# Kernel optimization log

Hardware: AMD Instinct MI355X
Metric: run time of the kernel (lower is better)

Reference implementation:

```python
import jax, jax.numpy as jnp
import numpy as np

D_KEY = 512
D_VALUE = 512
D_MEM_HIDDEN = 64
BATCH = 65536


def setup_inputs() -> dict:
    key = jax.random.key(0)
    ks = jax.random.split(key, 6)
    return {
        "key": jax.random.normal(ks[0], (BATCH, D_KEY), dtype=jnp.float32),
        "value": jax.random.normal(ks[1], (BATCH, D_VALUE), dtype=jnp.float32),
        # memory MLP weights (the stored memory)
        "mem_W1": jax.random.normal(ks[2], (D_MEM_HIDDEN, D_KEY), dtype=jnp.float32) * 0.02,
        "mem_b1": jnp.zeros((D_MEM_HIDDEN,), dtype=jnp.float32),
        "mem_W2": jax.random.normal(ks[3], (D_VALUE, D_MEM_HIDDEN), dtype=jnp.float32) * 0.02,
        "mem_b2": jnp.zeros((D_VALUE,), dtype=jnp.float32),
        # per-dimension precision head
        "prec_W": jax.random.normal(ks[4], (D_VALUE, D_KEY), dtype=jnp.float32) * 0.01,
        "prec_b": jnp.ones((D_VALUE,), dtype=jnp.float32),
    }


def reference(key, value, mem_W1, mem_b1, mem_W2, mem_b2, prec_W, prec_b):
    """Faithful translation of MemoryModule.free_energy.

    F = prec * clamp(value - pred, -3, 3)^2 - log(prec), averaged over d_value.
    """
    # predict: two-layer MLP with exact (erf) GELU, matching torch F.gelu default
    h = jax.nn.gelu(key @ mem_W1.T + mem_b1, approximate=False)  # (B, H)
    pred = h @ mem_W2.T + mem_b2                                  # (B, Dv)
    # precision head: softplus + 0.01, always positive
    prec = jax.nn.softplus(key @ prec_W.T + prec_b) + 0.01        # (B, Dv)
    error = jnp.clip(value - pred, -3.0, 3.0)                     # (B, Dv)
    F_per_dim = prec * error * error - jnp.log(prec)
    F_scalar = F_per_dim.mean(axis=-1)                            # (B,)
    return (F_scalar, pred, prec, error)
```

## Files before the change

kernel.cpp:

```cpp
#include <hip/hip_runtime.h>
#include <hip/hip_bf16.h>

#define BATCH 65536
#define DK 512
#define DV 512
#define DH 64
#define BMR 16

typedef __attribute__((ext_vector_type(8))) short bf16x8;
typedef __attribute__((ext_vector_type(4))) float f32x4;

__device__ __align__(16) short g_wb[327680];

__device__ __forceinline__ short f2bf(float f) {
    union { __hip_bfloat16 h; short s; } u;
    u.h = __float2bfloat16(f);
    return u.s;
}

__device__ __forceinline__ bf16x8 pack8(float4 a, float4 b) {
    bf16x8 r;
    r[0] = f2bf(a.x); r[1] = f2bf(a.y); r[2] = f2bf(a.z); r[3] = f2bf(a.w);
    r[4] = f2bf(b.x); r[5] = f2bf(b.y); r[6] = f2bf(b.z); r[7] = f2bf(b.w);
    return r;
}

__global__ __launch_bounds__(256) void conv_weights(
    const float* __restrict__ W1, const float* __restrict__ W2,
    const float* __restrict__ Wp)
{
    int f = blockIdx.x * 256 + threadIdx.x;
    int lane = f & 63;
    const float* src; int stride, row, col;
    if (f < 4096) {
        int t = f >> 10, kk = (f >> 6) & 15;
        src = W1; stride = DK;
        row = t * 16 + (lane & 15); col = kk * 32 + (lane >> 4) * 8;
    } else if (f < 8192) {
        int g = f - 4096; int t = g >> 7, kh = (g >> 6) & 1;
        src = W2; stride = DH;
        row = t * 16 + (lane & 15); col = kh * 32 + (lane >> 4) * 8;
    } else {
        int g = f - 8192; int t = g >> 10, kk = (g >> 6) & 15;
        src = Wp; stride = DK;
        row = t * 16 + (lane & 15); col = kk * 32 + (lane >> 4) * 8;
    }
    const float* p = src + (long)row * stride + col;
    float4 a = *reinterpret_cast<const float4*>(p);
    float4 b = *reinterpret_cast<const float4*>(p + 4);
    *reinterpret_cast<bf16x8*>(g_wb + (long)f * 8) = pack8(a, b);
}

#define KOF 0
#define XP  16384
#define XZ  24576

__global__ __launch_bounds__(256, 4) void fused_free_energy(
    const float* __restrict__ key, const float* __restrict__ value,
    const float* __restrict__ b1, const float* __restrict__ b2,
    const float* __restrict__ pb,
    float* __restrict__ outF, float* __restrict__ outPred,
    float* __restrict__ outPrec, float* __restrict__ outErr)
{
    __shared__ __align__(16) char lds[32768];

    const bf16x8* W1F = reinterpret_cast<const bf16x8*>(g_wb);
    const bf16x8* W2F = reinterpret_cast<const bf16x8*>(g_wb + 32768);
    const bf16x8* WpF = reinterpret_cast<const bf16x8*>(g_wb + 65536);

    const int tid  = threadIdx.x;
    const int wave = tid >> 6;
    const int lane = tid & 63;
    const int lh   = lane & 15;
    const int lg   = lane >> 4;
    const long row0 = (long)blockIdx.x * BMR;
    const f32x4 zf = {0.f, 0.f, 0.f, 0.f};

    {
        #pragma unroll
        for (int i = 0; i < 4; ++i) {
            int idx = i * 256 + tid;
            int r = idx >> 6, c8 = idx & 63;
            const float* p = key + (row0 + r) * DK + c8 * 8;
            float4 a = *reinterpret_cast<const float4*>(p);
            float4 b = *reinterpret_cast<const float4*>(p + 4);
            int byte = (r * 1024 + c8 * 16) ^ ((r & 7) << 4);
            *reinterpret_cast<bf16x8*>(lds + KOF + byte) = pack8(a, b);
        }
    }
    __syncthreads();

    #define KFRAG(kk) (*reinterpret_cast<const bf16x8*>( \
        lds + KOF + ((lh * 1024 + (kk) * 64 + lg * 16) ^ ((lh & 7) << 4))))

    bf16x8 hreg[2];
    {
        short hs_all[16];
        #pragma unroll
        for (int jt = 0; jt < 4; ++jt) {
            f32x4 aE = zf, aO = zf;
            #pragma unroll
            for (int kk = 0; kk < 16; kk += 2) {
                bf16x8 f0 = W1F[(jt * 16 + kk) * 64 + lane];
                bf16x8 f1 = W1F[(jt * 16 + kk + 1) * 64 + lane];
                aE = __builtin_amdgcn_mfma_f32_16x16x32_bf16(f0, KFRAG(kk),     aE, 0, 0, 0);
                aO = __builtin_amdgcn_mfma_f32_16x16x32_bf16(f1, KFRAG(kk + 1), aO, 0, 0, 0);
            }
            float4 b1v = *reinterpret_cast<const float4*>(b1 + jt * 16 + lg * 4);
            float b1a[4] = {b1v.x, b1v.y, b1v.z, b1v.w};
            #pragma unroll
            for (int r = 0; r < 4; ++r) {
                float z = aE[r] + aO[r] + b1a[r];
                float g = 0.5f * z * (1.0f + erff(z * 0.70710678f));
                hs_all[jt * 4 + r] = f2bf(g);
            }
        }
        #pragma unroll
        for (int jt = 0; jt < 4; ++jt) {
            int hb = XP + wave * 2048 + ((lh * 128 + jt * 32 + lg * 8) ^ ((lh & 7) << 4));
            short4 hv = {hs_all[jt * 4 + 0], hs_all[jt * 4 + 1],
                         hs_all[jt * 4 + 2], hs_all[jt * 4 + 3]};
            *reinterpret_cast<short4*>(lds + hb) = hv;
        }
        __syncthreads();
        #pragma unroll
        for (int kh = 0; kh < 2; ++kh) {
            int byte = (lh * 128 + kh * 64 + lg * 16) ^ ((lh & 7) << 4);
            hreg[kh] = *reinterpret_cast<const bf16x8*>(lds + XP + wave * 2048 + byte);
        }
        __syncthreads();
    }

    float facc0 = 0.f, facc1 = 0.f;
    #pragma unroll 1
    for (int ot = 0; ot < 4; ++ot) {
        #pragma unroll
        for (int sub = 0; sub < 2; ++sub) {
            const int tt = ot * 8 + wave * 2 + sub;
            f32x4 aE = zf, aO = zf;
            #pragma unroll
            for (int kk = 0; kk < 16; kk += 2) {
                bf16x8 f0 = WpF[(tt * 16 + kk) * 64 + lane];
                bf16x8 f1 = WpF[(tt * 16 + kk + 1) * 64 + lane];
                aE = __builtin_amdgcn_mfma_f32_16x16x32_bf16(f0, KFRAG(kk),     aE, 0, 0, 0);
                aO = __builtin_amdgcn_mfma_f32_16x16x32_bf16(f1, KFRAG(kk + 1), aO, 0, 0, 0);
            }
            f32x4 acc2 = zf;
            #pragma unroll
            for (int kh = 0; kh < 2; ++kh) {
                bf16x8 f = W2F[(tt * 2 + kh) * 64 + lane];
                acc2 = __builtin_amdgcn_mfma_f32_16x16x32_bf16(f, hreg[kh], acc2, 0, 0, 0);
            }
            int nb = tt * 16 + lg * 4;
            float4 b2v = *reinterpret_cast<const float4*>(b2 + nb);
            float4 pbv = *reinterpret_cast<const float4*>(pb + nb);
            f32x4 pz, zz;
            pz[0] = acc2[0] + b2v.x; pz[1] = acc2[1] + b2v.y;
            pz[2] = acc2[2] + b2v.z; pz[3] = acc2[3] + b2v.w;
            zz[0] = aE[0] + aO[0] + pbv.x; zz[1] = aE[1] + aO[1] + pbv.y;
            zz[2] = aE[2] + aO[2] + pbv.z; zz[3] = aE[3] + aO[3] + pbv.w;
            int relb = (wave * 2 + sub) * 64 + lg * 16;
            int sb = (lh * 512 + relb) ^ ((lh & 7) << 4);
            *reinterpret_cast<f32x4*>(lds + XP + sb) = pz;
            *reinterpret_cast<f32x4*>(lds + XZ + sb) = zz;
        }
        __syncthreads();

        #pragma unroll
        for (int ch = 0; ch < 2; ++ch) {
            int row  = wave * 4 + (lane >> 5) + ch * 2;
            int colb = (lane & 31) * 16;
            int rb   = (row * 512 + colb) ^ ((row & 7) << 4);
            float4 pr = *reinterpret_cast<const float4*>(lds + XP + rb);
            float4 zz = *reinterpret_cast<const float4*>(lds + XZ + rb);
            long ga = (row0 + row) * (long)DV + ot * 128 + (lane & 31) * 4;
            float4 va = *reinterpret_cast<const float4*>(value + ga);
            float pa[4] = {pr.x, pr.y, pr.z, pr.w};
            float za[4] = {zz.x, zz.y, zz.z, zz.w};
            float vaa[4] = {va.x, va.y, va.z, va.w};
            float er[4], pc[4], f = 0.f;
            #pragma unroll
            for (int r = 0; r < 4; ++r) {
                float z = za[r];
                float prec = fmaxf(z, 0.f) + __logf(1.0f + __expf(-fabsf(z))) + 0.01f;
                float e = fminf(fmaxf(vaa[r] - pa[r], -3.f), 3.f);
                pc[r] = prec; er[r] = e;
                f += prec * e * e - __logf(prec);
            }
            float4 pc4 = {pc[0], pc[1], pc[2], pc[3]};
            float4 er4 = {er[0], er[1], er[2], er[3]};
            *reinterpret_cast<float4*>(outPred + ga) = pr;
            *reinterpret_cast<float4*>(outPrec + ga) = pc4;
            *reinterpret_cast<float4*>(outErr  + ga) = er4;
            if (ch == 0) facc0 += f; else facc1 += f;
        }
        __syncthreads();
    }

    #pragma unroll
    for (int ch = 0; ch < 2; ++ch) {
        float s = (ch == 0) ? facc0 : facc1;
        #pragma unroll
        for (int off = 1; off < 32; off <<= 1)
            s += __shfl_xor(s, off, 64);
        if ((lane & 31) == 0)
            outF[row0 + wave * 4 + (lane >> 5) + ch * 2] = s * (1.0f / 512.0f);
    }
}

extern "C" void kernel_launch(void* const* d_in, const int* in_sizes, int n_in,
                              void* d_out, int out_size, void* d_ws, size_t ws_size,
                              hipStream_t stream) {
    const float* key   = (const float*)d_in[0];
    const float* value = (const float*)d_in[1];
    const float* W1    = (const float*)d_in[2];
    const float* b1    = (const float*)d_in[3];
    const float* W2    = (const float*)d_in[4];
    const float* b2    = (const float*)d_in[5];
    const float* Wp    = (const float*)d_in[6];
    const float* pb    = (const float*)d_in[7];

    float* outF    = (float*)d_out;
    float* outPred = outF + BATCH;
    float* outPrec = outPred + (long)BATCH * DV;
    float* outErr  = outPrec + (long)BATCH * DV;

    conv_weights<<<160, 256, 0, stream>>>(W1, W2, Wp);
    fused_free_energy<<<BATCH / BMR, 256, 0, stream>>>(key, value, b1, b2, pb,
                                                       outF, outPred, outPrec, outErr);
}
```

Measured before the change: 272.1 us.

## Prefetch value tiles one stage ahead and replace syncthreads with lighter barriers

Loads the value rows for the next output tile into registers before computing the current tile, so global load latency overlaps the MFMA work. The four-stage loop is fully unrolled with a double-buffered register prefetch. __syncthreads is replaced by an explicit s_waitcnt lgkmcnt(0) plus s_barrier, so barriers no longer wait on outstanding global memory operations. This uses more registers, and the barrier after the writeback has no explicit waitcnt, which relies on the LDS reads having already completed when their results were consumed.

```diff
diff --git a/kernel.cpp b/kernel.cpp
--- a/kernel.cpp
+++ b/kernel.cpp
@@ -9,6 +9,11 @@
 
 typedef __attribute__((ext_vector_type(8))) short bf16x8;
 typedef __attribute__((ext_vector_type(4))) float f32x4;
+
+#define LGKM_BAR() do { asm volatile("s_waitcnt lgkmcnt(0)" ::: "memory"); \
+                        __builtin_amdgcn_s_barrier(); } while (0)
+#define BAR()      do { asm volatile("" ::: "memory"); \
+                        __builtin_amdgcn_s_barrier(); } while (0)
 
 __device__ __align__(16) short g_wb[327680];
 
@@ -76,6 +81,18 @@
     const long row0 = (long)blockIdx.x * BMR;
     const f32x4 zf = {0.f, 0.f, 0.f, 0.f};
 
+    const int rowA  = wave * 4 + (lane >> 5);
+    const int colw  = (lane & 31) * 4;
+    const float* vbase0 = value + (row0 + rowA) * (long)DV + colw;
+    const float* vbase1 = vbase0 + 2 * DV;
+
+    float4 vA0, vA1, vB0, vB1;
+#define PREF(p, d0, d1) do { \
+        d0 = *reinterpret_cast<const float4*>(vbase0 + (p) * 128); \
+        d1 = *reinterpret_cast<const float4*>(vbase1 + (p) * 128); } while (0)
+
+    PREF(0, vA0, vA1);
+
     {
         #pragma unroll
         for (int i = 0; i < 4; ++i) {
@@ -88,7 +105,7 @@
             *reinterpret_cast<bf16x8*>(lds + KOF + byte) = pack8(a, b);
         }
     }
-    __syncthreads();
+    LGKM_BAR();
 
     #define KFRAG(kk) (*reinterpret_cast<const bf16x8*>( \
         lds + KOF + ((lh * 1024 + (kk) * 64 + lg * 16) ^ ((lh & 7) << 4))))
@@ -122,80 +139,92 @@
                          hs_all[jt * 4 + 2], hs_all[jt * 4 + 3]};
             *reinterpret_cast<short4*>(lds + hb) = hv;
         }
-        __syncthreads();
+        LGKM_BAR();
         #pragma unroll
         for (int kh = 0; kh < 2; ++kh) {
             int byte = (lh * 128 + kh * 64 + lg * 16) ^ ((lh & 7) << 4);
             hreg[kh] = *reinterpret_cast<const bf16x8*>(lds + XP + wave * 2048 + byte);
         }
-        __syncthreads();
+        LGKM_BAR();
     }
 
     float facc0 = 0.f, facc1 = 0.f;
-    #pragma unroll 1
-    for (int ot = 0; ot < 4; ++ot) {
-        #pragma unroll
-        for (int sub = 0; sub < 2; ++sub) {
-            const int tt = ot * 8 + wave * 2 + sub;
-            f32x4 aE = zf, aO = zf;
-            #pragma unroll
-            for (int kk = 0; kk < 16; kk += 2) {
-                bf16x8 f0 = WpF[(tt * 16 + kk) * 64 + lane];
-                bf16x8 f1 = WpF[(tt * 16 + kk + 1) * 64 + lane];
-                aE = __builtin_amdgcn_mfma_f32_16x16x32_bf16(f0, KFRAG(kk),     aE, 0, 0, 0);
-                aO = __builtin_amdgcn_mfma_f32_16x16x32_bf16(f1, KFRAG(kk + 1), aO, 0, 0, 0);
-            }
-            f32x4 acc2 = zf;
-            #pragma unroll
-            for (int kh = 0; kh < 2; ++kh) {
-                bf16x8 f = W2F[(tt * 2 + kh) * 64 + lane];
-                acc2 = __builtin_amdgcn_mfma_f32_16x16x32_bf16(f, hreg[kh], acc2, 0, 0, 0);
-            }
-            int nb = tt * 16 + lg * 4;
-            float4 b2v = *reinterpret_cast<const float4*>(b2 + nb);
-            float4 pbv = *reinterpret_cast<const float4*>(pb + nb);
-            f32x4 pz, zz;
-            pz[0] = acc2[0] + b2v.x; pz[1] = acc2[1] + b2v.y;
-            pz[2] = acc2[2] + b2v.z; pz[3] = acc2[3] + b2v.w;
-            zz[0] = aE[0] + aO[0] + pbv.x; zz[1] = aE[1] + aO[1] + pbv.y;
-            zz[2] = aE[2] + aO[2] + pbv.z; zz[3] = aE[3] + aO[3] + pbv.w;
-            int relb = (wave * 2 + sub) * 64 + lg * 16;
-            int sb = (lh * 512 + relb) ^ ((lh & 7) << 4);
-            *reinterpret_cast<f32x4*>(lds + XP + sb) = pz;
-            *reinterpret_cast<f32x4*>(lds + XZ + sb) = zz;
-        }
-        __syncthreads();
-
-        #pragma unroll
-        for (int ch = 0; ch < 2; ++ch) {
-            int row  = wave * 4 + (lane >> 5) + ch * 2;
-            int colb = (lane & 31) * 16;
-            int rb   = (row * 512 + colb) ^ ((row & 7) << 4);
-            float4 pr = *reinterpret_cast<const float4*>(lds + XP + rb);
-            float4 zz = *reinterpret_cast<const float4*>(lds + XZ + rb);
-            long ga = (row0 + row) * (long)DV + ot * 128 + (lane & 31) * 4;
-            float4 va = *reinterpret_cast<const float4*>(value + ga);
-            float pa[4] = {pr.x, pr.y, pr.z, pr.w};
-            float za[4] = {zz.x, zz.y, zz.z, zz.w};
-            float vaa[4] = {va.x, va.y, va.z, va.w};
-            float er[4], pc[4], f = 0.f;
-            #pragma unroll
-            for (int r = 0; r < 4; ++r) {
-                float z = za[r];
-                float prec = fmaxf(z, 0.f) + __logf(1.0f + __expf(-fabsf(z))) + 0.01f;
-                float e = fminf(fmaxf(vaa[r] - pa[r], -3.f), 3.f);
-                pc[r] = prec; er[r] = e;
-                f += prec * e * e - __logf(prec);
-            }
-            float4 pc4 = {pc[0], pc[1], pc[2], pc[3]};
-            float4 er4 = {er[0], er[1], er[2], er[3]};
-            *reinterpret_cast<float4*>(outPred + ga) = pr;
-            *reinterpret_cast<float4*>(outPrec + ga) = pc4;
-            *reinterpret_cast<float4*>(outErr  + ga) = er4;
-            if (ch == 0) facc0 += f; else facc1 += f;
-        }
-        __syncthreads();
-    }
+
+#define COMPUTE(ot) do {                                                          \
+        _Pragma("unroll")                                                         \
+        for (int sub = 0; sub < 2; ++sub) {                                       \
+            const int tt = (ot) * 8 + wave * 2 + sub;                             \
+            f32x4 aE = zf, aO = zf;                                               \
+            _Pragma("unroll")                                                     \
+            for (int kk = 0; kk < 16; kk += 2) {                                  \
+                bf16x8 f0 = WpF[(tt * 16 + kk) * 64 + lane];                      \
+                bf16x8 f1 = WpF[(tt * 16 + kk + 1) * 64 + lane];                  \
+                aE = __builtin_amdgcn_mfma_f32_16x16x32_bf16(f0, KFRAG(kk),     aE, 0, 0, 0); \
+                aO = __builtin_amdgcn_mfma_f32_16x16x32_bf16(f1, KFRAG(kk + 1), aO, 0, 0, 0); \
+            }                                                                     \
+            f32x4 acc2 = zf;                                                      \
+            _Pragma("unroll")                                                     \
+            for (int kh = 0; kh < 2; ++kh) {                                      \
+                bf16x8 f = W2F[(tt * 2 + kh) * 64 + lane];                        \
+                acc2 = __builtin_amdgcn_mfma_f32_16x16x32_bf16(f, hreg[kh], acc2, 0, 0, 0); \
+            }                                                                     \
+            int nb = tt * 16 + lg * 4;                                            \
+            float4 b2v = *reinterpret_cast<const float4*>(b2 + nb);               \
+            float4 pbv = *reinterpret_cast<const float4*>(pb + nb);               \
+            f32x4 pz, zz;                                                         \
+            pz[0] = acc2[0] + b2v.x; pz[1] = acc2[1] + b2v.y;                     \
+            pz[2] = acc2[2] + b2v.z; pz[3] = acc2[3] + b2v.w;                     \
+            zz[0] = aE[0] + aO[0] + pbv.x; zz[1] = aE[1] + aO[1] + pbv.y;         \
+            zz[2] = aE[2] + aO[2] + pbv.z; zz[3] = aE[3] + aO[3] + pbv.w;         \
+            int relb = (wave * 2 + sub) * 64 + lg * 16;                           \
+            int sb = (lh * 512 + relb) ^ ((lh & 7) << 4);                         \
+            *reinterpret_cast<f32x4*>(lds + XP + sb) = pz;                        \
+            *reinterpret_cast<f32x4*>(lds + XZ + sb) = zz;                        \
+        }                                                                         \
+    } while (0)
+
+#define WRITEBACK(ot, v0, v1) do {                                                \
+        _Pragma("unroll")                                                         \
+        for (int ch = 0; ch < 2; ++ch) {                                          \
+            int row  = rowA + ch * 2;                                             \
+            int colb = (lane & 31) * 16;                                          \
+            int rb   = (row * 512 + colb) ^ ((row & 7) << 4);                     \
+            float4 pr = *reinterpret_cast<const float4*>(lds + XP + rb);          \
+            float4 zv = *reinterpret_cast<const float4*>(lds + XZ + rb);          \
+            long ga = (row0 + row) * (long)DV + (ot) * 128 + colw;                \
+            float4 va = (ch == 0) ? (v0) : (v1);                                  \
+            float pa[4]  = {pr.x, pr.y, pr.z, pr.w};                              \
+            float za[4]  = {zv.x, zv.y, zv.z, zv.w};                              \
+            float vaa[4] = {va.x, va.y, va.z, va.w};                              \
+            float er[4], pc[4], f = 0.f;                                          \
+            _Pragma("unroll")                                                     \
+            for (int r = 0; r < 4; ++r) {                                         \
+                float z = za[r];                                                  \
+                float prec = fmaxf(z, 0.f) + __logf(1.0f + __expf(-fabsf(z))) + 0.01f; \
+                float e = fminf(fmaxf(vaa[r] - pa[r], -3.f), 3.f);                \
+                pc[r] = prec; er[r] = e;                                          \
+                f += prec * e * e - __logf(prec);                                 \
+            }                                                                     \
+            float4 pc4 = {pc[0], pc[1], pc[2], pc[3]};                            \
+            float4 er4 = {er[0], er[1], er[2], er[3]};                            \
+            *reinterpret_cast<float4*>(outPred + ga) = pr;                        \
+            *reinterpret_cast<float4*>(outPrec + ga) = pc4;                       \
+            *reinterpret_cast<float4*>(outErr  + ga) = er4;                       \
+            if (ch == 0) facc0 += f; else facc1 += f;                             \
+        }                                                                         \
+    } while (0)
+
+    COMPUTE(0); PREF(1, vB0, vB1); LGKM_BAR();
+    WRITEBACK(0, vA0, vA1); BAR();
+
+    COMPUTE(1); PREF(2, vA0, vA1); LGKM_BAR();
+    WRITEBACK(1, vB0, vB1); BAR();
+
+    COMPUTE(2); PREF(3, vB0, vB1); LGKM_BAR();
+    WRITEBACK(2, vA0, vA1); BAR();
+
+    COMPUTE(3); LGKM_BAR();
+    WRITEBACK(3, vB0, vB1);
 
     #pragma unroll
     for (int ch = 0; ch < 2; ++ch) {
@@ -204,7 +233,7 @@
         for (int off = 1; off < 32; off <<= 1)
             s += __shfl_xor(s, off, 64);
         if ((lane & 31) == 0)
-            outF[row0 + wave * 4 + (lane >> 5) + ch * 2] = s * (1.0f / 512.0f);
+            outF[row0 + rowA + ch * 2] = s * (1.0f / 512.0f);
     }
 }
 
```

Measured after the change: 261.3 us. 1.04x faster.

## Double row tile to 32 so each weight fragment feeds two MFMAs

Applied to the files above, without the earlier changes.

Raises the block row tile from 16 to 32 rows. Each loaded precision-head and W2 weight fragment is now reused across two M-tiles, which halves the global or L2 weight traffic per row. The W1/GELU stage runs on only two waves, the value loads are hoisted to the top of each phase, plain barriers are replaced with an lgkmcnt-wait plus s_barrier, and the final F reduction now goes through LDS. The cost is more LDS per block (48KB) and an occupancy hint lowered to 3 blocks per CU, with half the waves idle during the hidden-layer stage.

```diff
diff --git a/kernel.cpp b/kernel.cpp
--- a/kernel.cpp
+++ b/kernel.cpp
@@ -5,10 +5,13 @@
 #define DK 512
 #define DV 512
 #define DH 64
-#define BMR 16
+#define BMR 32
 
 typedef __attribute__((ext_vector_type(8))) short bf16x8;
 typedef __attribute__((ext_vector_type(4))) float f32x4;
+
+#define LGKM_BAR() do { asm volatile("s_waitcnt lgkmcnt(0)" ::: "memory"); \
+                        __builtin_amdgcn_s_barrier(); } while (0)
 
 __device__ __align__(16) short g_wb[327680];
 
@@ -52,17 +55,17 @@
 }
 
 #define KOF 0
-#define XP  16384
-#define XZ  24576
-
-__global__ __launch_bounds__(256, 4) void fused_free_energy(
+#define XP  32768
+#define XZ  40960
+
+__global__ __launch_bounds__(256, 3) void fused_free_energy(
     const float* __restrict__ key, const float* __restrict__ value,
     const float* __restrict__ b1, const float* __restrict__ b2,
     const float* __restrict__ pb,
     float* __restrict__ outF, float* __restrict__ outPred,
     float* __restrict__ outPrec, float* __restrict__ outErr)
 {
-    __shared__ __align__(16) char lds[32768];
+    __shared__ __align__(16) char lds[49152];
 
     const bf16x8* W1F = reinterpret_cast<const bf16x8*>(g_wb);
     const bf16x8* W2F = reinterpret_cast<const bf16x8*>(g_wb + 32768);
@@ -76,26 +79,27 @@
     const long row0 = (long)blockIdx.x * BMR;
     const f32x4 zf = {0.f, 0.f, 0.f, 0.f};
 
-    {
-        #pragma unroll
-        for (int i = 0; i < 4; ++i) {
-            int idx = i * 256 + tid;
-            int r = idx >> 6, c8 = idx & 63;
-            const float* p = key + (row0 + r) * DK + c8 * 8;
-            float4 a = *reinterpret_cast<const float4*>(p);
-            float4 b = *reinterpret_cast<const float4*>(p + 4);
-            int byte = (r * 1024 + c8 * 16) ^ ((r & 7) << 4);
-            *reinterpret_cast<bf16x8*>(lds + KOF + byte) = pack8(a, b);
-        }
-    }
-    __syncthreads();
-
-    #define KFRAG(kk) (*reinterpret_cast<const bf16x8*>( \
-        lds + KOF + ((lh * 1024 + (kk) * 64 + lg * 16) ^ ((lh & 7) << 4))))
-
-    bf16x8 hreg[2];
-    {
-        short hs_all[16];
+    const int rw = tid >> 4;
+    const int cw = (tid & 15) * 4;
+    const float* vrow0 = value + (row0 + rw) * (long)DV + cw;
+    const float* vrow1 = vrow0 + 16 * (long)DV;
+
+    #pragma unroll
+    for (int i = 0; i < 8; ++i) {
+        int idx = i * 256 + tid;
+        int r = idx >> 6, c8 = idx & 63;
+        const float* p = key + (row0 + r) * DK + c8 * 8;
+        float4 a = *reinterpret_cast<const float4*>(p);
+        float4 b = *reinterpret_cast<const float4*>(p + 4);
+        int byte = (r * 1024 + c8 * 16) ^ ((r & 7) << 4);
+        *reinterpret_cast<bf16x8*>(lds + KOF + byte) = pack8(a, b);
+    }
+    LGKM_BAR();
+
+    #define KFRAG(mt, kk) (*reinterpret_cast<const bf16x8*>( \
+        lds + KOF + (((mt) * 16384 + lh * 1024 + (kk) * 64 + lg * 16) ^ ((lh & 7) << 4))))
+
+    if (wave < 2) {
         #pragma unroll
         for (int jt = 0; jt < 4; ++jt) {
             f32x4 aE = zf, aO = zf;
@@ -103,80 +107,94 @@
             for (int kk = 0; kk < 16; kk += 2) {
                 bf16x8 f0 = W1F[(jt * 16 + kk) * 64 + lane];
                 bf16x8 f1 = W1F[(jt * 16 + kk + 1) * 64 + lane];
-                aE = __builtin_amdgcn_mfma_f32_16x16x32_bf16(f0, KFRAG(kk),     aE, 0, 0, 0);
-                aO = __builtin_amdgcn_mfma_f32_16x16x32_bf16(f1, KFRAG(kk + 1), aO, 0, 0, 0);
+                aE = __builtin_amdgcn_mfma_f32_16x16x32_bf16(f0, KFRAG(wave, kk),     aE, 0, 0, 0);
+                aO = __builtin_amdgcn_mfma_f32_16x16x32_bf16(f1, KFRAG(wave, kk + 1), aO, 0, 0, 0);
             }
             float4 b1v = *reinterpret_cast<const float4*>(b1 + jt * 16 + lg * 4);
             float b1a[4] = {b1v.x, b1v.y, b1v.z, b1v.w};
+            short hs[4];
             #pragma unroll
             for (int r = 0; r < 4; ++r) {
                 float z = aE[r] + aO[r] + b1a[r];
                 float g = 0.5f * z * (1.0f + erff(z * 0.70710678f));
-                hs_all[jt * 4 + r] = f2bf(g);
+                hs[r] = f2bf(g);
             }
-        }
-        #pragma unroll
-        for (int jt = 0; jt < 4; ++jt) {
             int hb = XP + wave * 2048 + ((lh * 128 + jt * 32 + lg * 8) ^ ((lh & 7) << 4));
-            short4 hv = {hs_all[jt * 4 + 0], hs_all[jt * 4 + 1],
-                         hs_all[jt * 4 + 2], hs_all[jt * 4 + 3]};
+            short4 hv = {hs[0], hs[1], hs[2], hs[3]};
             *reinterpret_cast<short4*>(lds + hb) = hv;
         }
-        __syncthreads();
+    }
+    LGKM_BAR();
+    bf16x8 hreg[2][2];
+    #pragma unroll
+    for (int mt = 0; mt < 2; ++mt)
         #pragma unroll
         for (int kh = 0; kh < 2; ++kh) {
             int byte = (lh * 128 + kh * 64 + lg * 16) ^ ((lh & 7) << 4);
-            hreg[kh] = *reinterpret_cast<const bf16x8*>(lds + XP + wave * 2048 + byte);
-        }
-        __syncthreads();
-    }
+            hreg[mt][kh] = *reinterpret_cast<const bf16x8*>(lds + XP + mt * 2048 + byte);
+        }
+    LGKM_BAR();
 
     float facc0 = 0.f, facc1 = 0.f;
+
     #pragma unroll 1
-    for (int ot = 0; ot < 4; ++ot) {
-        #pragma unroll
-        for (int sub = 0; sub < 2; ++sub) {
-            const int tt = ot * 8 + wave * 2 + sub;
-            f32x4 aE = zf, aO = zf;
-            #pragma unroll
-            for (int kk = 0; kk < 16; kk += 2) {
-                bf16x8 f0 = WpF[(tt * 16 + kk) * 64 + lane];
-                bf16x8 f1 = WpF[(tt * 16 + kk + 1) * 64 + lane];
-                aE = __builtin_amdgcn_mfma_f32_16x16x32_bf16(f0, KFRAG(kk),     aE, 0, 0, 0);
-                aO = __builtin_amdgcn_mfma_f32_16x16x32_bf16(f1, KFRAG(kk + 1), aO, 0, 0, 0);
-            }
-            f32x4 acc2 = zf;
-            #pragma unroll
-            for (int kh = 0; kh < 2; ++kh) {
-                bf16x8 f = W2F[(tt * 2 + kh) * 64 + lane];
-                acc2 = __builtin_amdgcn_mfma_f32_16x16x32_bf16(f, hreg[kh], acc2, 0, 0, 0);
-            }
-            int nb = tt * 16 + lg * 4;
-            float4 b2v = *reinterpret_cast<const float4*>(b2 + nb);
-            float4 pbv = *reinterpret_cast<const float4*>(pb + nb);
+    for (int ph = 0; ph < 8; ++ph) {
+        float4 va0 = *reinterpret_cast<const float4*>(vrow0 + ph * 64);
+        float4 va1 = *reinterpret_cast<const float4*>(vrow1 + ph * 64);
+
+        const int tt = ph * 4 + wave;
+        f32x4 a0 = zf, a1 = zf;
+        #pragma unroll
+        for (int kk = 0; kk < 16; ++kk) {
+            bf16x8 f0 = WpF[(tt * 16 + kk) * 64 + lane];
+            a0 = __builtin_amdgcn_mfma_f32_16x16x32_bf16(f0, KFRAG(0, kk), a0, 0, 0, 0);
+            a1 = __builtin_amdgcn_mfma_f32_16x16x32_bf16(f0, KFRAG(1, kk), a1, 0, 0, 0);
+        }
+        f32x4 c0 = zf, c1 = zf;
+        #pragma unroll
+        for (int kh = 0; kh < 2; ++kh) {
+            bf16x8 f = W2F[(tt * 2 + kh) * 64 + lane];
+            c0 = __builtin_amdgcn_mfma_f32_16x16x32_bf16(f, hreg[0][kh], c0, 0, 0, 0);
+            c1 = __builtin_amdgcn_mfma_f32_16x16x32_bf16(f, hreg[1][kh], c1, 0, 0, 0);
+        }
+
+        int nb = tt * 16 + lg * 4;
+        float4 b2v = *reinterpret_cast<const float4*>(b2 + nb);
+        float4 pbv = *reinterpret_cast<const float4*>(pb + nb);
+
+        {
             f32x4 pz, zz;
-            pz[0] = acc2[0] + b2v.x; pz[1] = acc2[1] + b2v.y;
-            pz[2] = acc2[2] + b2v.z; pz[3] = acc2[3] + b2v.w;
-            zz[0] = aE[0] + aO[0] + pbv.x; zz[1] = aE[1] + aO[1] + pbv.y;
-            zz[2] = aE[2] + aO[2] + pbv.z; zz[3] = aE[3] + aO[3] + pbv.w;
-            int relb = (wave * 2 + sub) * 64 + lg * 16;
-            int sb = (lh * 512 + relb) ^ ((lh & 7) << 4);
+            pz[0] = c0[0] + b2v.x; pz[1] = c0[1] + b2v.y;
+            pz[2] = c0[2] + b2v.z; pz[3] = c0[3] + b2v.w;
+            zz[0] = a0[0] + pbv.x; zz[1] = a0[1] + pbv.y;
+            zz[2] = a0[2] + pbv.z; zz[3] = a0[3] + pbv.w;
+            int sb = (lh * 256 + wave * 64 + lg * 16) ^ ((lh & 7) << 4);
             *reinterpret_cast<f32x4*>(lds + XP + sb) = pz;
             *reinterpret_cast<f32x4*>(lds + XZ + sb) = zz;
         }
-        __syncthreads();
+        {
+            f32x4 pz, zz;
+            pz[0] = c1[0] + b2v.x; pz[1] = c1[1] + b2v.y;
+            pz[2] = c1[2] + b2v.z; pz[3] = c1[3] + b2v.w;
+            zz[0] = a1[0] + pbv.x; zz[1] = a1[1] + pbv.y;
+            zz[2] = a1[2] + pbv.z; zz[3] = a1[3] + pbv.w;
+            int row = 16 + lh;
+            int sb = (row * 256 + wave * 64 + lg * 16) ^ ((row & 7) << 4);
+            *reinterpret_cast<f32x4*>(lds + XP + sb) = pz;
+            *reinterpret_cast<f32x4*>(lds + XZ + sb) = zz;
+        }
+        LGKM_BAR();
 
         #pragma unroll
         for (int ch = 0; ch < 2; ++ch) {
-            int row  = wave * 4 + (lane >> 5) + ch * 2;
-            int colb = (lane & 31) * 16;
-            int rb   = (row * 512 + colb) ^ ((row & 7) << 4);
+            int row = rw + ch * 16;
+            int rb  = (row * 256 + cw * 4) ^ ((row & 7) << 4);
             float4 pr = *reinterpret_cast<const float4*>(lds + XP + rb);
-            float4 zz = *reinterpret_cast<const float4*>(lds + XZ + rb);
-            long ga = (row0 + row) * (long)DV + ot * 128 + (lane & 31) * 4;
-            float4 va = *reinterpret_cast<const float4*>(value + ga);
-            float pa[4] = {pr.x, pr.y, pr.z, pr.w};
-            float za[4] = {zz.x, zz.y, zz.z, zz.w};
+            float4 zv = *reinterpret_cast<const float4*>(lds + XZ + rb);
+            long ga = (row0 + row) * (long)DV + ph * 64 + cw;
+            float4 va = (ch == 0) ? va0 : va1;
+            float pa[4]  = {pr.x, pr.y, pr.z, pr.w};
+            float za[4]  = {zv.x, zv.y, zv.z, zv.w};
             float vaa[4] = {va.x, va.y, va.z, va.w};
             float er[4], pc[4], f = 0.f;
             #pragma unroll
@@ -194,17 +212,19 @@
             *reinterpret_cast<float4*>(outErr  + ga) = er4;
             if (ch == 0) facc0 += f; else facc1 += f;
         }
-        __syncthreads();
-    }
-
-    #pragma unroll
-    for (int ch = 0; ch < 2; ++ch) {
-        float s = (ch == 0) ? facc0 : facc1;
-        #pragma unroll
-        for (int off = 1; off < 32; off <<= 1)
-            s += __shfl_xor(s, off, 64);
-        if ((lane & 31) == 0)
-            outF[row0 + wave * 4 + (lane >> 5) + ch * 2] = s * (1.0f / 512.0f);
+        LGKM_BAR();
+    }
+
+    float* fpart = reinterpret_cast<float*>(lds + XP);
+    fpart[rw * 16 + (tid & 15)]        = facc0;
+    fpart[(rw + 16) * 16 + (tid & 15)] = facc1;
+    __syncthreads();
+    if (tid < 32) {
+        const float* p = fpart + tid * 16;
+        float s = 0.f;
+        #pragma unroll
+        for (int i = 0; i < 16; ++i) s += p[i];
+        outF[row0 + tid] = s * (1.0f / 512.0f);
     }
 }
 
```

Result: faster. 249.5 us (-8.3%).
